# Kernel tuning notes

Hardware: AMD Instinct MI355X
Metric: run time of the kernel (lower is better)

## Reference

```python
import jax, jax.numpy as jnp
import numpy as np

N_NODES = 70000
N_EDGES = 800000
IN_SAGE = 1024
FEAT_CH = 128
EXTRA = 20
HIDDEN = (FEAT_CH + EXTRA) // 4  # 37
OUT = 3
BN_EPS = 1e-5


def setup_inputs() -> dict:
    key = jax.random.key(0)
    ks = jax.random.split(key, 12)
    features = jax.random.normal(ks[0], (N_NODES, 1044), dtype=jnp.float32)
    edges = jax.random.randint(ks[1], (2, N_EDGES), 0, N_NODES, dtype=jnp.int32)
    edges2 = jax.random.randint(ks[2], (2, N_EDGES), 0, N_NODES, dtype=jnp.int32)
    edge_features = jax.random.normal(ks[3], (N_EDGES, 1), dtype=jnp.float32)
    s = 1.0 / np.sqrt(IN_SAGE)
    w_sage_l = jax.random.uniform(ks[4], (FEAT_CH, IN_SAGE), jnp.float32, -s, s)
    b_sage_l = jax.random.uniform(ks[5], (FEAT_CH,), jnp.float32, -s, s)
    w_sage_r = jax.random.uniform(ks[6], (FEAT_CH, IN_SAGE), jnp.float32, -s, s)
    s1 = 1.0 / np.sqrt(FEAT_CH + EXTRA)
    fc1_w = jax.random.uniform(ks[7], (HIDDEN, FEAT_CH + EXTRA), jnp.float32, -s1, s1)
    fc1_b = jax.random.uniform(ks[8], (HIDDEN,), jnp.float32, -s1, s1)
    s2 = 1.0 / np.sqrt(HIDDEN)
    fc2_w = jax.random.uniform(ks[9], (OUT, HIDDEN), jnp.float32, -s2, s2)
    fc2_b = jax.random.uniform(ks[10], (OUT,), jnp.float32, -s2, s2)
    bn_gamma = jnp.ones((HIDDEN,), jnp.float32)
    bn_beta = jnp.zeros((HIDDEN,), jnp.float32)
    bn_mean = jnp.zeros((HIDDEN,), jnp.float32)
    bn_var = jnp.ones((HIDDEN,), jnp.float32)
    return dict(features=features, edges=edges, edges2=edges2, edge_features=edge_features,
                w_sage_l=w_sage_l, b_sage_l=b_sage_l, w_sage_r=w_sage_r,
                fc1_w=fc1_w, fc1_b=fc1_b, fc2_w=fc2_w, fc2_b=fc2_b,
                bn_gamma=bn_gamma, bn_beta=bn_beta, bn_mean=bn_mean, bn_var=bn_var)


def reference(features, edges, edges2, edge_features,
              w_sage_l, b_sage_l, w_sage_r,
              fc1_w, fc1_b, fc2_w, fc2_b,
              bn_gamma, bn_beta, bn_mean, bn_var):
    n = features.shape[0]
    x_in = features[:, :IN_SAGE]            # [N, 1024]
    src, dst = edges[0], edges[1]
    # SAGEConv mean aggregation: mean of source-node features per destination node
    agg = jax.ops.segment_sum(x_in[src], dst, num_segments=n)          # [N, 1024]
    cnt = jax.ops.segment_sum(jnp.ones_like(dst, jnp.float32), dst, num_segments=n)
    mean = agg / jnp.maximum(cnt, 1.0)[:, None]
    # lin_l(aggr) + lin_r(x)  (PyG SAGEConv, root_weight=True, bias on lin_l)
    x = mean @ w_sage_l.T + b_sage_l + x_in @ w_sage_r.T               # [N, 128]
    x = jax.nn.relu(x)                                                 # activation; dropout is identity in eval
    x = jnp.concatenate([x, features[:, IN_SAGE:]], axis=1)            # [N, 148]
    x = jax.nn.relu(x @ fc1_w.T + fc1_b)                               # [N, 37]
    x = (x - bn_mean) * jax.lax.rsqrt(bn_var + BN_EPS) * bn_gamma + bn_beta  # BatchNorm1d eval
    return x @ fc2_w.T + fc2_b                                         # [N, 3]
```

## Files before the change

### kernel.cpp

```cpp
#include <hip/hip_runtime.h>

#define N_NODES 70000
#define N_EDGES 800000
#define ROWLEN  1044
#define KDIM    1024
#define FEAT    128
#define NOUT    256
#define HIDDEN  37
#define CIN     148
#define NCHUNK  69

typedef __attribute__((ext_vector_type(8))) short short8;
typedef __attribute__((ext_vector_type(4))) float f32x4;

static __device__ __forceinline__ unsigned short f2bf(float f) {
  unsigned int u = __float_as_uint(f);
  u += 0x7FFF + ((u >> 16) & 1);
  return (unsigned short)(u >> 16);
}
static __device__ __forceinline__ float bf2f(unsigned int u) {
  return __uint_as_float(u << 16);
}

__global__ __launch_bounds__(256) void cvt_w(
    const float* __restrict__ wl, const float* __restrict__ wr,
    unsigned short* __restrict__ wbf)
{
  const int i = blockIdx.x * 256 + threadIdx.x;
  const int half = (FEAT * KDIM) / 4;
  const float* src = (i < half) ? wl : wr;
  const int j = (i < half) ? i : (i - half);
  const float4 v = ((const float4*)src)[j];
  ushort4 u = make_ushort4(f2bf(v.x), f2bf(v.y), f2bf(v.z), f2bf(v.w));
  ((ushort4*)wbf)[i] = u;
}

__global__ __launch_bounds__(256) void hist(
    const int* __restrict__ edges, unsigned int* __restrict__ cnt)
{
  const int e = blockIdx.x * 256 + threadIdx.x;
  atomicAdd(&cnt[edges[N_EDGES + e]], 1u);
}

__global__ __launch_bounds__(256) void scan_a(
    const unsigned int* __restrict__ cnt, unsigned int* __restrict__ partial)
{
  __shared__ unsigned int s[256];
  const int t = threadIdx.x;
  const int base = blockIdx.x * 1024 + t * 4;
  unsigned int sum = 0;
  #pragma unroll
  for (int j = 0; j < 4; j++) sum += (base + j < N_NODES) ? cnt[base + j] : 0u;
  s[t] = sum; __syncthreads();
  for (int off = 128; off > 0; off >>= 1) {
    if (t < off) s[t] += s[t + off];
    __syncthreads();
  }
  if (t == 0) partial[blockIdx.x] = s[0];
}

__global__ __launch_bounds__(128) void scan_b(
    const unsigned int* __restrict__ partial, unsigned int* __restrict__ chunk_off)
{
  __shared__ unsigned int s[128];
  const int t = threadIdx.x;
  const unsigned int own = (t < NCHUNK) ? partial[t] : 0u;
  s[t] = own; __syncthreads();
  for (int off = 1; off < 128; off <<= 1) {
    unsigned int x = (t >= off) ? s[t - off] : 0u;
    __syncthreads();
    s[t] += x;
    __syncthreads();
  }
  if (t < NCHUNK) chunk_off[t] = s[t] - own;
}

__global__ __launch_bounds__(256) void scan_c(
    const unsigned int* __restrict__ cnt, const unsigned int* __restrict__ chunk_off,
    unsigned int* __restrict__ row_start)
{
  __shared__ unsigned int s[256];
  const int t = threadIdx.x;
  const int base = blockIdx.x * 1024 + t * 4;
  unsigned int v[4], sum = 0;
  #pragma unroll
  for (int j = 0; j < 4; j++) { v[j] = (base + j < N_NODES) ? cnt[base + j] : 0u; sum += v[j]; }
  s[t] = sum; __syncthreads();
  for (int off = 1; off < 256; off <<= 1) {
    unsigned int x = (t >= off) ? s[t - off] : 0u;
    __syncthreads();
    s[t] += x;
    __syncthreads();
  }
  unsigned int run = chunk_off[blockIdx.x] + (s[t] - sum);
  #pragma unroll
  for (int j = 0; j < 4; j++) {
    if (base + j < N_NODES) row_start[base + j] = run;
    run += v[j];
  }
}

__global__ __launch_bounds__(256) void fill_csr(
    const int* __restrict__ edges, const unsigned int* __restrict__ row_start,
    unsigned int* __restrict__ wc, int* __restrict__ col)
{
  const int e = blockIdx.x * 256 + threadIdx.x;
  const int src = edges[e];
  const int dst = edges[N_EDGES + e];
  const unsigned int pos = row_start[dst] + atomicAdd(&wc[dst], 1u);
  col[pos] = src;
}

__global__ __launch_bounds__(256, 2) void gemm_sage(
    const float* __restrict__ feat,
    const unsigned short* __restrict__ wbf,
    unsigned short* __restrict__ y)
{
  __shared__ __align__(16) unsigned short As[128][72];
  __shared__ __align__(16) unsigned short Bs[256][72];

  const int tid  = threadIdx.x;
  const int lane = tid & 63;
  const int wid  = tid >> 6;
  const int wm   = (wid & 1) * 64;
  const int wn   = (wid >> 1) * 128;
  const int m0   = blockIdx.x * 128;

  f32x4 acc[4][8];
  const f32x4 zero = {0.f, 0.f, 0.f, 0.f};
  #pragma unroll
  for (int i = 0; i < 4; i++)
    #pragma unroll
    for (int j = 0; j < 8; j++) acc[i][j] = zero;

  const int c4  = tid & 15;
  const int r0  = tid >> 4;
  const int c8  = tid & 7;
  const int r0b = tid >> 3;

  for (int kk = 0; kk < KDIM; kk += 64) {
    #pragma unroll
    for (int i = 0; i < 8; i++) {
      int r = r0 + 16 * i;
      int m = m0 + r; if (m >= N_NODES) m = N_NODES - 1;
      const float4 v = *(const float4*)(feat + (size_t)m * ROWLEN + kk + c4 * 4);
      ushort4 u = make_ushort4(f2bf(v.x), f2bf(v.y), f2bf(v.z), f2bf(v.w));
      *(ushort4*)&As[r][c4 * 4] = u;
    }
    #pragma unroll
    for (int i = 0; i < 8; i++) {
      int r = r0b + 32 * i;
      const uint4 v = *(const uint4*)(wbf + (size_t)r * KDIM + kk + c8 * 8);
      *(uint4*)&Bs[r][c8 * 8] = v;
    }
    __syncthreads();
    #pragma unroll
    for (int s = 0; s < 2; s++) {
      const int colk = s * 32 + (lane >> 4) * 8;
      const int row  = lane & 15;
      short8 a[4], b[8];
      #pragma unroll
      for (int t = 0; t < 4; t++) a[t] = *(const short8*)&As[wm + t * 16 + row][colk];
      #pragma unroll
      for (int t = 0; t < 8; t++) b[t] = *(const short8*)&Bs[wn + t * 16 + row][colk];
      #pragma unroll
      for (int i = 0; i < 4; i++)
        #pragma unroll
        for (int j = 0; j < 8; j++)
          acc[i][j] = __builtin_amdgcn_mfma_f32_16x16x32_bf16(a[i], b[j], acc[i][j], 0, 0, 0);
    }
    __syncthreads();
  }

  const int mb = m0 + wm + (lane >> 4) * 4;
  const int nb = wn + (lane & 15);
  #pragma unroll
  for (int i = 0; i < 4; i++) {
    #pragma unroll
    for (int r = 0; r < 4; r++) {
      const int m = mb + i * 16 + r;
      if (m < N_NODES) {
        #pragma unroll
        for (int j = 0; j < 8; j++)
          y[(size_t)m * NOUT + nb + j * 16] = f2bf(acc[i][j][r]);
      }
    }
  }
}

__global__ __launch_bounds__(256) void gather_epilogue(
    const float* __restrict__ feat,
    const unsigned short* __restrict__ y,
    const unsigned int* __restrict__ row_start,
    const unsigned int* __restrict__ cnt,
    const int* __restrict__ col,
    const float* __restrict__ b_sage_l,
    const float* __restrict__ fc1_w, const float* __restrict__ fc1_b,
    const float* __restrict__ fc2_w, const float* __restrict__ fc2_b,
    const float* __restrict__ bn_gamma, const float* __restrict__ bn_beta,
    const float* __restrict__ bn_mean, const float* __restrict__ bn_var,
    float* __restrict__ out)
{
  __shared__ float w1t[CIN][HIDDEN + 1];
  __shared__ float vbuf[4][CIN];
  __shared__ float hbuf[4][HIDDEN + 3];
  const int tid  = threadIdx.x;
  const int lane = tid & 63;
  const int w    = tid >> 6;

  for (int i = tid; i < HIDDEN * CIN; i += 256) {
    const int j = i / CIN;
    const int c = i - j * CIN;
    w1t[c][j] = fc1_w[i];
  }
  __syncthreads();

  const int m = blockIdx.x * 4 + w;
  const int e0 = (int)row_start[m];
  const int n  = (int)cnt[m];

  float s0 = 0.f, s1 = 0.f;
  int i = 0;
  for (; i + 2 <= n; i += 2) {
    const int sa = col[e0 + i];
    const int sb = col[e0 + i + 1];
    const unsigned int va = *(const unsigned int*)(y + (size_t)sa * NOUT + lane * 2);
    const unsigned int vb = *(const unsigned int*)(y + (size_t)sb * NOUT + lane * 2);
    s0 += bf2f(va & 0xFFFFu) + bf2f(vb & 0xFFFFu);
    s1 += bf2f(va >> 16)     + bf2f(vb >> 16);
  }
  if (i < n) {
    const int sa = col[e0 + i];
    const unsigned int va = *(const unsigned int*)(y + (size_t)sa * NOUT + lane * 2);
    s0 += bf2f(va & 0xFFFFu);
    s1 += bf2f(va >> 16);
  }

  const float inv = 1.0f / fmaxf((float)n, 1.0f);
  const unsigned int vr = *(const unsigned int*)(y + (size_t)m * NOUT + FEAT + lane * 2);
  vbuf[w][2 * lane]     = fmaxf(s0 * inv + b_sage_l[2 * lane]     + bf2f(vr & 0xFFFFu), 0.0f);
  vbuf[w][2 * lane + 1] = fmaxf(s1 * inv + b_sage_l[2 * lane + 1] + bf2f(vr >> 16),     0.0f);
  if (lane < CIN - FEAT)
    vbuf[w][FEAT + lane] = feat[(size_t)m * ROWLEN + KDIM + lane];
  __syncthreads();

  if (lane < HIDDEN) {
    float h = fc1_b[lane];
    #pragma unroll 4
    for (int c = 0; c < CIN; c++) h += w1t[c][lane] * vbuf[w][c];
    h = fmaxf(h, 0.0f);
    h = (h - bn_mean[lane]) * rsqrtf(bn_var[lane] + 1e-5f) * bn_gamma[lane] + bn_beta[lane];
    hbuf[w][lane] = h;
  }
  __syncthreads();

  if (lane < 3) {
    float o = fc2_b[lane];
    #pragma unroll
    for (int j = 0; j < HIDDEN; j++) o += fc2_w[lane * HIDDEN + j] * hbuf[w][j];
    out[(size_t)m * 3 + lane] = o;
  }
}

#define Y_OFF    0u
#define Y_BYTES  (N_NODES * NOUT * 2u)
#define WBF_OFF  Y_BYTES
#define WBF_BYTES (NOUT * KDIM * 2u)
#define CNT_OFF  (WBF_OFF + WBF_BYTES)
#define CNT_BYTES (N_NODES * 4u)
#define WC_OFF   (CNT_OFF + CNT_BYTES)
#define RS_OFF   (WC_OFF + CNT_BYTES)
#define PART_OFF (RS_OFF + CNT_BYTES)
#define COFF_OFF (PART_OFF + 512u)
#define COL_OFF  (COFF_OFF + 512u)
#define COL_BYTES (N_EDGES * 4u)

extern "C" void kernel_launch(void* const* d_in, const int* in_sizes, int n_in,
                              void* d_out, int out_size, void* d_ws, size_t ws_size,
                              hipStream_t stream) {
  const float* feat     = (const float*)d_in[0];
  const int*   edges    = (const int*)  d_in[1];
  const float* w_sage_l = (const float*)d_in[4];
  const float* b_sage_l = (const float*)d_in[5];
  const float* w_sage_r = (const float*)d_in[6];
  const float* fc1_w    = (const float*)d_in[7];
  const float* fc1_b    = (const float*)d_in[8];
  const float* fc2_w    = (const float*)d_in[9];
  const float* fc2_b    = (const float*)d_in[10];
  const float* bn_gamma = (const float*)d_in[11];
  const float* bn_beta  = (const float*)d_in[12];
  const float* bn_mean  = (const float*)d_in[13];
  const float* bn_var   = (const float*)d_in[14];
  float* out = (float*)d_out;

  char* ws = (char*)d_ws;
  unsigned short* y    = (unsigned short*)(ws + Y_OFF);
  unsigned short* wbf  = (unsigned short*)(ws + WBF_OFF);
  unsigned int*   cnt  = (unsigned int*)(ws + CNT_OFF);
  unsigned int*   wc   = (unsigned int*)(ws + WC_OFF);
  unsigned int*   rs   = (unsigned int*)(ws + RS_OFF);
  unsigned int*   part = (unsigned int*)(ws + PART_OFF);
  unsigned int*   coff = (unsigned int*)(ws + COFF_OFF);
  int*            col  = (int*)(ws + COL_OFF);

  (void)hipMemsetAsync(ws + CNT_OFF, 0, 2u * CNT_BYTES, stream);
  cvt_w<<<256, 256, 0, stream>>>(w_sage_l, w_sage_r, wbf);
  hist<<<N_EDGES / 256, 256, 0, stream>>>(edges, cnt);
  scan_a<<<NCHUNK, 256, 0, stream>>>(cnt, part);
  scan_b<<<1, 128, 0, stream>>>(part, coff);
  scan_c<<<NCHUNK, 256, 0, stream>>>(cnt, coff, rs);
  fill_csr<<<N_EDGES / 256, 256, 0, stream>>>(edges, rs, wc, col);
  gemm_sage<<<(N_NODES + 127) / 128, 256, 0, stream>>>(feat, wbf, y);
  gather_epilogue<<<N_NODES / 4, 256, 0, stream>>>(feat, y, rs, cnt, col, b_sage_l,
                                                   fc1_w, fc1_b, fc2_w, fc2_b,
                                                   bn_gamma, bn_beta, bn_mean, bn_var, out);
}
```

Baseline: 697.1 us.

## Shrink GEMM M tile to 96, raise occupancy, fuse memset into weight conversion

New measurement: 683.9 us. No clear change (-1.9%).

```diff
diff --git a/kernel.cpp b/kernel.cpp
--- a/kernel.cpp
+++ b/kernel.cpp
@@ -1,4 +1,5 @@
 #include <hip/hip_runtime.h>
+#include <hip/hip_bf16.h>
 
 #define N_NODES 70000
 #define N_EDGES 800000
@@ -9,6 +10,7 @@
 #define HIDDEN  37
 #define CIN     148
 #define NCHUNK  69
+#define TM      96
 
 typedef __attribute__((ext_vector_type(8))) short short8;
 typedef __attribute__((ext_vector_type(4))) float f32x4;
@@ -21,18 +23,24 @@
 static __device__ __forceinline__ float bf2f(unsigned int u) {
   return __uint_as_float(u << 16);
 }
+static __device__ __forceinline__ unsigned int pk2bf(float a, float b) {
+  union { __hip_bfloat162 h; unsigned int u; } cv;
+  cv.h = __float22bfloat162_rn(float2{a, b});
+  return cv.u;
+}
 
 __global__ __launch_bounds__(256) void cvt_w(
     const float* __restrict__ wl, const float* __restrict__ wr,
-    unsigned short* __restrict__ wbf)
+    unsigned short* __restrict__ wbf, unsigned int* __restrict__ z)
 {
   const int i = blockIdx.x * 256 + threadIdx.x;
   const int half = (FEAT * KDIM) / 4;
   const float* src = (i < half) ? wl : wr;
   const int j = (i < half) ? i : (i - half);
   const float4 v = ((const float4*)src)[j];
-  ushort4 u = make_ushort4(f2bf(v.x), f2bf(v.y), f2bf(v.z), f2bf(v.w));
-  ((ushort4*)wbf)[i] = u;
+  uint2 u = make_uint2(pk2bf(v.x, v.y), pk2bf(v.z, v.w));
+  ((uint2*)wbf)[i] = u;
+  for (int k = i; k < 2 * N_NODES; k += 65536) z[k] = 0u;
 }
 
 __global__ __launch_bounds__(256) void hist(
@@ -111,25 +119,25 @@
   col[pos] = src;
 }
 
-__global__ __launch_bounds__(256, 2) void gemm_sage(
+__global__ __launch_bounds__(256, 3) void gemm_sage(
     const float* __restrict__ feat,
     const unsigned short* __restrict__ wbf,
     unsigned short* __restrict__ y)
 {
-  __shared__ __align__(16) unsigned short As[128][72];
+  __shared__ __align__(16) unsigned short As[TM][72];
   __shared__ __align__(16) unsigned short Bs[256][72];
 
   const int tid  = threadIdx.x;
   const int lane = tid & 63;
   const int wid  = tid >> 6;
-  const int wm   = (wid & 1) * 64;
+  const int wm   = (wid & 1) * 48;
   const int wn   = (wid >> 1) * 128;
-  const int m0   = blockIdx.x * 128;
-
-  f32x4 acc[4][8];
+  const int m0   = blockIdx.x * TM;
+
+  f32x4 acc[3][8];
   const f32x4 zero = {0.f, 0.f, 0.f, 0.f};
   #pragma unroll
-  for (int i = 0; i < 4; i++)
+  for (int i = 0; i < 3; i++)
     #pragma unroll
     for (int j = 0; j < 8; j++) acc[i][j] = zero;
 
@@ -140,12 +148,12 @@
 
   for (int kk = 0; kk < KDIM; kk += 64) {
     #pragma unroll
-    for (int i = 0; i < 8; i++) {
+    for (int i = 0; i < 6; i++) {
       int r = r0 + 16 * i;
       int m = m0 + r; if (m >= N_NODES) m = N_NODES - 1;
       const float4 v = *(const float4*)(feat + (size_t)m * ROWLEN + kk + c4 * 4);
-      ushort4 u = make_ushort4(f2bf(v.x), f2bf(v.y), f2bf(v.z), f2bf(v.w));
-      *(ushort4*)&As[r][c4 * 4] = u;
+      uint2 u = make_uint2(pk2bf(v.x, v.y), pk2bf(v.z, v.w));
+      *(uint2*)&As[r][c4 * 4] = u;
     }
     #pragma unroll
     for (int i = 0; i < 8; i++) {
@@ -158,16 +166,16 @@
     for (int s = 0; s < 2; s++) {
       const int colk = s * 32 + (lane >> 4) * 8;
       const int row  = lane & 15;
-      short8 a[4], b[8];
+      short8 a[3];
       #pragma unroll
-      for (int t = 0; t < 4; t++) a[t] = *(const short8*)&As[wm + t * 16 + row][colk];
+      for (int t = 0; t < 3; t++) a[t] = *(const short8*)&As[wm + t * 16 + row][colk];
       #pragma unroll
-      for (int t = 0; t < 8; t++) b[t] = *(const short8*)&Bs[wn + t * 16 + row][colk];
-      #pragma unroll
-      for (int i = 0; i < 4; i++)
+      for (int j = 0; j < 8; j++) {
+        const short8 b = *(const short8*)&Bs[wn + j * 16 + row][colk];
         #pragma unroll
-        for (int j = 0; j < 8; j++)
-          acc[i][j] = __builtin_amdgcn_mfma_f32_16x16x32_bf16(a[i], b[j], acc[i][j], 0, 0, 0);
+        for (int t = 0; t < 3; t++)
+          acc[t][j] = __builtin_amdgcn_mfma_f32_16x16x32_bf16(a[t], b, acc[t][j], 0, 0, 0);
+      }
     }
     __syncthreads();
   }
@@ -175,14 +183,14 @@
   const int mb = m0 + wm + (lane >> 4) * 4;
   const int nb = wn + (lane & 15);
   #pragma unroll
-  for (int i = 0; i < 4; i++) {
+  for (int t = 0; t < 3; t++) {
     #pragma unroll
     for (int r = 0; r < 4; r++) {
-      const int m = mb + i * 16 + r;
+      const int m = mb + t * 16 + r;
       if (m < N_NODES) {
         #pragma unroll
         for (int j = 0; j < 8; j++)
-          y[(size_t)m * NOUT + nb + j * 16] = f2bf(acc[i][j][r]);
+          y[(size_t)m * NOUT + nb + j * 16] = f2bf(acc[t][j][r]);
       }
     }
   }
@@ -221,15 +229,19 @@
 
   float s0 = 0.f, s1 = 0.f;
   int i = 0;
-  for (; i + 2 <= n; i += 2) {
+  for (; i + 4 <= n; i += 4) {
     const int sa = col[e0 + i];
     const int sb = col[e0 + i + 1];
+    const int sc = col[e0 + i + 2];
+    const int sd = col[e0 + i + 3];
     const unsigned int va = *(const unsigned int*)(y + (size_t)sa * NOUT + lane * 2);
     const unsigned int vb = *(const unsigned int*)(y + (size_t)sb * NOUT + lane * 2);
-    s0 += bf2f(va & 0xFFFFu) + bf2f(vb & 0xFFFFu);
-    s1 += bf2f(va >> 16)     + bf2f(vb >> 16);
-  }
-  if (i < n) {
+    const unsigned int vc = *(const unsigned int*)(y + (size_t)sc * NOUT + lane * 2);
+    const unsigned int vd = *(const unsigned int*)(y + (size_t)sd * NOUT + lane * 2);
+    s0 += (bf2f(va & 0xFFFFu) + bf2f(vb & 0xFFFFu)) + (bf2f(vc & 0xFFFFu) + bf2f(vd & 0xFFFFu));
+    s1 += (bf2f(va >> 16)     + bf2f(vb >> 16))     + (bf2f(vc >> 16)     + bf2f(vd >> 16));
+  }
+  for (; i < n; i++) {
     const int sa = col[e0 + i];
     const unsigned int va = *(const unsigned int*)(y + (size_t)sa * NOUT + lane * 2);
     s0 += bf2f(va & 0xFFFFu);
@@ -303,14 +315,13 @@
   unsigned int*   coff = (unsigned int*)(ws + COFF_OFF);
   int*            col  = (int*)(ws + COL_OFF);
 
-  (void)hipMemsetAsync(ws + CNT_OFF, 0, 2u * CNT_BYTES, stream);
-  cvt_w<<<256, 256, 0, stream>>>(w_sage_l, w_sage_r, wbf);
+  cvt_w<<<256, 256, 0, stream>>>(w_sage_l, w_sage_r, wbf, cnt);
   hist<<<N_EDGES / 256, 256, 0, stream>>>(edges, cnt);
   scan_a<<<NCHUNK, 256, 0, stream>>>(cnt, part);
   scan_b<<<1, 128, 0, stream>>>(part, coff);
   scan_c<<<NCHUNK, 256, 0, stream>>>(cnt, coff, rs);
   fill_csr<<<N_EDGES / 256, 256, 0, stream>>>(edges, rs, wc, col);
-  gemm_sage<<<(N_NODES + 127) / 128, 256, 0, stream>>>(feat, wbf, y);
+  gemm_sage<<<(N_NODES + TM - 1) / TM, 256, 0, stream>>>(feat, wbf, y);
   gather_epilogue<<<N_NODES / 4, 256, 0, stream>>>(feat, y, rs, cnt, col, b_sage_l,
                                                    fc1_w, fc1_b, fc2_w, fc2_b,
                                                    bn_gamma, bn_beta, bn_mean, bn_var, out);
```
